# Kernel optimization log

Hardware: AMD Instinct MI355X
Metric: run time of the kernel (lower is better)

The kernel has to match this reference:

```python
import jax, jax.numpy as jnp
import numpy as np

N = 50000        # num_nodes
E = 800000       # num_edges (before self-loops)
F_IN = 64        # node_feature_dim
HID = 128        # hidden_dim per head (layer 1)
HEADS = 4
OUT = 256        # output_dim (layer 2, heads=1)
NEG_SLOPE = 0.2  # PyG GATConv default leaky_relu slope


def setup_inputs() -> dict:
    key = jax.random.key(0)
    ks = jax.random.split(key, 10)
    edge_index = jax.random.randint(ks[0], (2, E), 0, N, dtype=jnp.int32)
    node_emb = jax.random.normal(ks[1], (N, F_IN), jnp.float32)
    # Layer 1: GATConv(64 -> 128, heads=4, concat=True)
    W1 = jax.random.normal(ks[2], (F_IN, HEADS * HID), jnp.float32) / np.sqrt(F_IN)
    a_src1 = jax.random.normal(ks[3], (HEADS, HID), jnp.float32) / np.sqrt(HID)
    a_dst1 = jax.random.normal(ks[4], (HEADS, HID), jnp.float32) / np.sqrt(HID)
    b1 = jnp.zeros((HEADS * HID,), jnp.float32)
    # Layer 2: GATConv(512 -> 256, heads=1)
    W2 = jax.random.normal(ks[5], (HEADS * HID, OUT), jnp.float32) / np.sqrt(HEADS * HID)
    a_src2 = jax.random.normal(ks[6], (1, OUT), jnp.float32) / np.sqrt(OUT)
    a_dst2 = jax.random.normal(ks[7], (1, OUT), jnp.float32) / np.sqrt(OUT)
    b2 = jnp.zeros((OUT,), jnp.float32)
    return {
        "edge_index": edge_index, "node_emb": node_emb,
        "W1": W1, "a_src1": a_src1, "a_dst1": a_dst1, "b1": b1,
        "W2": W2, "a_src2": a_src2, "a_dst2": a_dst2, "b2": b2,
        "batch_size": 1,
    }


def gat_layer(x, src, dst, W, a_src, a_dst, b, heads, ch):
    """PyG-style GATConv (concat=True, self-loops already in src/dst)."""
    n = x.shape[0]
    xw = (x @ W).reshape(n, heads, ch)                       # [N, H, C]
    alpha_s = jnp.einsum('nhc,hc->nh', xw, a_src)            # [N, H]
    alpha_d = jnp.einsum('nhc,hc->nh', xw, a_dst)            # [N, H]
    logits = jax.nn.leaky_relu(alpha_s[src] + alpha_d[dst], NEG_SLOPE)  # [Etot, H]
    # numerically stable segment softmax over edges grouped by dst
    m = jax.ops.segment_max(logits, dst, num_segments=n)     # [N, H]
    e = jnp.exp(logits - m[dst])                             # [Etot, H]
    denom = jax.ops.segment_sum(e, dst, num_segments=n)      # [N, H]
    alpha = e / denom[dst]                                   # [Etot, H]
    msg = xw[src] * alpha[:, :, None]                        # [Etot, H, C]
    out = jax.ops.segment_sum(msg, dst, num_segments=n)      # [N, H, C]
    return out.reshape(n, heads * ch) + b


def reference(edge_index, node_emb, W1, a_src1, a_dst1, b1,
              W2, a_src2, a_dst2, b2, batch_size):
    # PyG GATConv adds self-loops by default
    loop = jnp.arange(N, dtype=edge_index.dtype)
    src = jnp.concatenate([edge_index[0], loop])
    dst = jnp.concatenate([edge_index[1], loop])
    x = gat_layer(node_emb, src, dst, W1, a_src1, a_dst1, b1, HEADS, HID)
    x = jax.nn.elu(x)                                        # dropout = identity (eval)
    x = gat_layer(x, src, dst, W2, a_src2, a_dst2, b2, 1, OUT)
    g = jnp.mean(x, axis=0, keepdims=True)                   # [1, OUT]
    if batch_size > 1:
        g = jnp.broadcast_to(g, (batch_size, OUT))
    return g
```

## Files before the change

kernel.cpp:

```cpp
#include <hip/hip_runtime.h>
#include <cstdint>
#include <cstddef>

#define NEG_SLOPE 0.2f

typedef __bf16 bf16x8 __attribute__((ext_vector_type(8)));
typedef __bf16 bf16x4 __attribute__((ext_vector_type(4)));
typedef float f32x4 __attribute__((ext_vector_type(4)));

__device__ __forceinline__ int dstKeyOf(const int* ei, int E, int i) {
  return (i < E) ? ei[E + i] : (i - E);
}
__device__ __forceinline__ int srcKeyOf(const int* ei, int E, int i) {
  return (i < E) ? ei[i] : (i - E);
}

__global__ __launch_bounds__(256) void prep_all_kernel(
    const float* __restrict__ W1, const float* __restrict__ as1, const float* __restrict__ ad1,
    const float* __restrict__ W2, const float* __restrict__ as2, const float* __restrict__ ad2,
    float* __restrict__ Vs, float* __restrict__ Vd,
    float* __restrict__ vs2, float* __restrict__ vd2,
    __bf16* __restrict__ W1T) {
  int bid = blockIdx.x, tid = threadIdx.x;
  if (bid == 0) {
    int k = tid >> 2, h = tid & 3;
    const float* w = W1 + k * 512 + h * 128;
    const float* a1 = as1 + h * 128;
    const float* a2 = ad1 + h * 128;
    float s = 0.f, d = 0.f;
    for (int c = 0; c < 128; ++c) { float wv = w[c]; s += wv * a1[c]; d += wv * a2[c]; }
    Vs[k * 4 + h] = s; Vd[k * 4 + h] = d;
  } else if (bid <= 2) {
    int k = (bid - 1) * 256 + tid;
    if (k < 512) {
      const float* w = W2 + k * 256;
      float s = 0.f, d = 0.f;
      for (int c = 0; c < 256; ++c) { float wv = w[c]; s += wv * as2[c]; d += wv * ad2[c]; }
      vs2[k] = s; vd2[k] = d;
    }
  } else {
    int idx = (bid - 3) * 256 + tid;
    int n = idx >> 6, k = idx & 63;
    W1T[idx] = (__bf16)W1[(size_t)k * 512 + n];
  }
}

__global__ void emb_prep_kernel(const float* __restrict__ emb, const float* __restrict__ Vs,
                                const float* __restrict__ Vd, __bf16* __restrict__ embb,
                                float* __restrict__ as_, float* __restrict__ ad_, int n) {
  __shared__ float sVs[256];
  __shared__ float sVd[256];
  for (int i = threadIdx.x; i < 256; i += blockDim.x) { sVs[i] = Vs[i]; sVd[i] = Vd[i]; }
  __syncthreads();
  int node = blockIdx.x * blockDim.x + threadIdx.x;
  if (node >= n) return;
  const float* xr = emb + (size_t)node * 64;
  __bf16* br = embb + (size_t)node * 64;
  float accs[4] = {}, accd[4] = {};
  for (int k = 0; k < 64; k += 4) {
    float4 xv = *(const float4*)(xr + k);
    bf16x4 o;
    o[0] = (__bf16)xv.x; o[1] = (__bf16)xv.y; o[2] = (__bf16)xv.z; o[3] = (__bf16)xv.w;
    *(bf16x4*)(br + k) = o;
#pragma unroll
    for (int h = 0; h < 4; ++h) {
      accs[h] += xv.x * sVs[(k + 0) * 4 + h] + xv.y * sVs[(k + 1) * 4 + h] +
                 xv.z * sVs[(k + 2) * 4 + h] + xv.w * sVs[(k + 3) * 4 + h];
      accd[h] += xv.x * sVd[(k + 0) * 4 + h] + xv.y * sVd[(k + 1) * 4 + h] +
                 xv.z * sVd[(k + 2) * 4 + h] + xv.w * sVd[(k + 3) * 4 + h];
    }
  }
#pragma unroll
  for (int h = 0; h < 4; ++h) {
    as_[(size_t)node * 4 + h] = accs[h];
    ad_[(size_t)node * 4 + h] = accd[h];
  }
}

__global__ __launch_bounds__(256) void hist_kernel(const int* __restrict__ ei, int E, int NT,
                                                   int nblk, int* __restrict__ hist) {
  __shared__ int h[256];
  int tid = threadIdx.x;
  h[tid] = 0;
  __syncthreads();
  int sec = (int)blockIdx.x >= nblk;
  int blk = blockIdx.x - sec * nblk;
  int base = blk * 1024;
#pragma unroll
  for (int j = 0; j < 4; ++j) {
    int i = base + j * 256 + tid;
    if (i < NT) {
      int key = sec ? srcKeyOf(ei, E, i) : dstKeyOf(ei, E, i);
      atomicAdd(&h[key >> 8], 1);
    }
  }
  __syncthreads();
  hist[(size_t)(sec * 256 + tid) * nblk + blk] = h[tid];
}

__global__ __launch_bounds__(1024) void exscan1_kernel(int* __restrict__ a, int* __restrict__ bsum,
                                                       int M) {
  __shared__ int ws[16];
  int t = threadIdx.x, lane = t & 63, w = t >> 6;
  int i = blockIdx.x * 1024 + t;
  int v = (i < M) ? a[i] : 0;
  int x = v;
#pragma unroll
  for (int s = 1; s < 64; s <<= 1) {
    int tt = __shfl_up(x, s, 64);
    if (lane >= s) x += tt;
  }
  if (lane == 63) ws[w] = x;
  __syncthreads();
  int wo = 0;
  for (int k = 0; k < w; ++k) wo += ws[k];
  if (i < M) a[i] = wo + x - v;
  if (t == 1023) bsum[blockIdx.x] = wo + x;
}

__global__ __launch_bounds__(512) void exscan2_kernel(int* __restrict__ bsum, int nb) {
  __shared__ int buf[512];
  int t = threadIdx.x;
  int v = (t < nb) ? bsum[t] : 0;
  buf[t] = v;
  __syncthreads();
  for (int s = 1; s < 512; s <<= 1) {
    int x = (t >= s) ? buf[t - s] : 0;
    __syncthreads();
    buf[t] += x;
    __syncthreads();
  }
  if (t < nb) bsum[t] = buf[t] - v;
}

__global__ __launch_bounds__(1024) void exscan3_kernel(int* __restrict__ a,
                                                       const int* __restrict__ bsum, int M) {
  int i = blockIdx.x * 1024 + threadIdx.x;
  if (i < M) a[i] += bsum[blockIdx.x];
}

__global__ __launch_bounds__(256) void scatter1_kernel(const int* __restrict__ ei, int E, int NT,
                                                       int nblk, const int* __restrict__ scanned,
                                                       int2* __restrict__ p1buf) {
  __shared__ int bins[256];
  int tid = threadIdx.x;
  int sec = (int)blockIdx.x >= nblk;
  int blk = blockIdx.x - sec * nblk;
  bins[tid] = scanned[(size_t)(sec * 256 + tid) * nblk + blk];
  __syncthreads();
  int base = blk * 1024;
#pragma unroll
  for (int j = 0; j < 4; ++j) {
    int i = base + j * 256 + tid;
    if (i < NT) {
      int k, p;
      if (sec == 0) { k = dstKeyOf(ei, E, i); p = srcKeyOf(ei, E, i); }
      else          { k = srcKeyOf(ei, E, i); p = dstKeyOf(ei, E, i); }
      int pos = atomicAdd(&bins[k >> 8], 1);
      p1buf[pos] = make_int2(k, p);
    }
  }
}

__global__ __launch_bounds__(1024) void sortlow_kernel(const int* __restrict__ scanned,
                                                       const int2* __restrict__ p1buf,
                                                       int nblk, int NT,
                                                       int* __restrict__ keyD, int* __restrict__ srcD,
                                                       int* __restrict__ keyS, int* __restrict__ dstS) {
  __shared__ int h[256];
  __shared__ int b2[256];
  int tid = threadIdx.x;
  int w = blockIdx.x;
  int sec = w >= 256;
  int d0 = w - sec * 256;
  int beg = scanned[(size_t)(sec * 256 + d0) * nblk];
  int end = (w == 511) ? 2 * NT : scanned[(size_t)(sec * 256 + d0 + 1) * nblk];
  if (tid < 256) h[tid] = 0;
  __syncthreads();
  for (int i = beg + tid; i < end; i += 1024) atomicAdd(&h[p1buf[i].x & 255], 1);
  __syncthreads();
  if (tid < 256) b2[tid] = h[tid];
  __syncthreads();
  for (int s = 1; s < 256; s <<= 1) {
    int x = (tid >= s && tid < 256) ? b2[tid - s] : 0;
    __syncthreads();
    if (tid < 256) b2[tid] += x;
    __syncthreads();
  }
  if (tid < 256) b2[tid] = beg + b2[tid] - h[tid];
  __syncthreads();
  for (int i = beg + tid; i < end; i += 1024) {
    int2 it = p1buf[i];
    int pos = atomicAdd(&b2[it.x & 255], 1);
    if (sec == 0) { keyD[pos] = it.x; srcD[pos] = it.y; }
    else          { keyS[pos - NT] = it.x; dstS[pos - NT] = it.y; }
  }
}

__global__ void bounds_kernel(const int* __restrict__ keyD, const int* __restrict__ keyS,
                              int* __restrict__ off, int* __restrict__ offS, int NT, int n) {
  int x = blockIdx.x * 256 + threadIdx.x;
  if (x == 0) { off[n] = NT; offS[n] = NT; }
  if (x >= 2 * n) return;
  int sec = x >= n;
  int d = x - sec * n;
  const int* key = sec ? keyS : keyD;
  int lo = 0, hi = NT;
  while (lo < hi) {
    int mid = (lo + hi) >> 1;
    if (key[mid] < d) lo = mid + 1; else hi = mid;
  }
  if (sec) offS[d] = lo; else off[d] = lo;
}

__global__ __launch_bounds__(128) void agg_emb_kernel(
    const int* __restrict__ off, const int* __restrict__ csr_src,
    const __bf16* __restrict__ embb, const float* __restrict__ as_,
    const float* __restrict__ ad_, __bf16* __restrict__ aggE) {
  int d = blockIdx.x * 2 + (threadIdx.x >> 6);
  int lane = threadIdx.x & 63;
  int g = lane >> 4, p = lane & 15;
  float4 adv = *(const float4*)(ad_ + (size_t)d * 4);
  float acc[4][4] = {};
  float wsum[4] = {};
  int beg = off[d], end = off[d + 1];
  for (int i0 = beg; i0 < end; i0 += 8) {
    int iA = i0 + g, iB = i0 + 4 + g;
    int idxA = (iA < end) ? iA : (end - 1);
    int idxB = (iB < end) ? iB : (end - 1);
    float vmA = (iA < end) ? 1.f : 0.f;
    float vmB = (iB < end) ? 1.f : 0.f;
    int sA = csr_src[idxA];
    int sB = csr_src[idxB];
    float4 aA = *(const float4*)(as_ + (size_t)sA * 4);
    float4 aB = *(const float4*)(as_ + (size_t)sB * 4);
    bf16x4 vA = *(const bf16x4*)(embb + (size_t)sA * 64 + p * 4);
    bf16x4 vB = *(const bf16x4*)(embb + (size_t)sB * 64 + p * 4);
    float lA0 = aA.x + adv.x; lA0 = lA0 >= 0.f ? lA0 : NEG_SLOPE * lA0;
    float lA1 = aA.y + adv.y; lA1 = lA1 >= 0.f ? lA1 : NEG_SLOPE * lA1;
    float lA2 = aA.z + adv.z; lA2 = lA2 >= 0.f ? lA2 : NEG_SLOPE * lA2;
    float lA3 = aA.w + adv.w; lA3 = lA3 >= 0.f ? lA3 : NEG_SLOPE * lA3;
    float lB0 = aB.x + adv.x; lB0 = lB0 >= 0.f ? lB0 : NEG_SLOPE * lB0;
    float lB1 = aB.y + adv.y; lB1 = lB1 >= 0.f ? lB1 : NEG_SLOPE * lB1;
    float lB2 = aB.z + adv.z; lB2 = lB2 >= 0.f ? lB2 : NEG_SLOPE * lB2;
    float lB3 = aB.w + adv.w; lB3 = lB3 >= 0.f ? lB3 : NEG_SLOPE * lB3;
    float wA0 = __expf(lA0) * vmA, wA1 = __expf(lA1) * vmA;
    float wA2 = __expf(lA2) * vmA, wA3 = __expf(lA3) * vmA;
    float wB0 = __expf(lB0) * vmB, wB1 = __expf(lB1) * vmB;
    float wB2 = __expf(lB2) * vmB, wB3 = __expf(lB3) * vmB;
    float fA0 = (float)vA[0], fA1 = (float)vA[1], fA2 = (float)vA[2], fA3 = (float)vA[3];
    float fB0 = (float)vB[0], fB1 = (float)vB[1], fB2 = (float)vB[2], fB3 = (float)vB[3];
    acc[0][0] += wA0 * fA0; acc[0][1] += wA0 * fA1; acc[0][2] += wA0 * fA2; acc[0][3] += wA0 * fA3;
    acc[1][0] += wA1 * fA0; acc[1][1] += wA1 * fA1; acc[1][2] += wA1 * fA2; acc[1][3] += wA1 * fA3;
    acc[2][0] += wA2 * fA0; acc[2][1] += wA2 * fA1; acc[2][2] += wA2 * fA2; acc[2][3] += wA2 * fA3;
    acc[3][0] += wA3 * fA0; acc[3][1] += wA3 * fA1; acc[3][2] += wA3 * fA2; acc[3][3] += wA3 * fA3;
    acc[0][0] += wB0 * fB0; acc[0][1] += wB0 * fB1; acc[0][2] += wB0 * fB2; acc[0][3] += wB0 * fB3;
    acc[1][0] += wB1 * fB0; acc[1][1] += wB1 * fB1; acc[1][2] += wB1 * fB2; acc[1][3] += wB1 * fB3;
    acc[2][0] += wB2 * fB0; acc[2][1] += wB2 * fB1; acc[2][2] += wB2 * fB2; acc[2][3] += wB2 * fB3;
    acc[3][0] += wB3 * fB0; acc[3][1] += wB3 * fB1; acc[3][2] += wB3 * fB2; acc[3][3] += wB3 * fB3;
    wsum[0] += wA0 + wB0; wsum[1] += wA1 + wB1; wsum[2] += wA2 + wB2; wsum[3] += wA3 + wB3;
  }
#pragma unroll
  for (int h = 0; h < 4; ++h) {
#pragma unroll
    for (int c = 0; c < 4; ++c) {
      acc[h][c] += __shfl_xor(acc[h][c], 16, 64);
      acc[h][c] += __shfl_xor(acc[h][c], 32, 64);
    }
    wsum[h] += __shfl_xor(wsum[h], 16, 64);
    wsum[h] += __shfl_xor(wsum[h], 32, 64);
  }
  if (g == 0) {
#pragma unroll
    for (int h = 0; h < 4; ++h) {
      float inv = 1.0f / wsum[h];
      bf16x4 o;
      o[0] = (__bf16)(acc[h][0] * inv); o[1] = (__bf16)(acc[h][1] * inv);
      o[2] = (__bf16)(acc[h][2] * inv); o[3] = (__bf16)(acc[h][3] * inv);
      *(bf16x4*)(aggE + (size_t)d * 256 + h * 64 + p * 4) = o;
    }
  }
}

__global__ __launch_bounds__(256) void gemm1p_kernel(const __bf16* __restrict__ aggE,
                                                     const __bf16* __restrict__ W1T,
                                                     const float* __restrict__ b1,
                                                     const float* __restrict__ vs2,
                                                     const float* __restrict__ vd2,
                                                     __bf16* __restrict__ x1,
                                                     float* __restrict__ as2p,
                                                     float* __restrict__ ad2p, int M) {
  __shared__ __bf16 Asl[128 * 72];
  __shared__ __bf16 Bsl[128 * 72];
  int tid = threadIdx.x;
  int h = blockIdx.z;
  int m0 = blockIdx.x * 128;
  int wave = tid >> 6, lane = tid & 63;
  int wm = (wave >> 1) * 64, wn = (wave & 1) * 64;
  int l15 = lane & 15, kg = lane >> 4;
#pragma unroll
  for (int i = 0; i < 4; ++i) {
    int c = tid + i * 256;
    int row = c >> 3, off = (c & 7) * 8;
    bf16x8 va = {};
    int gr = m0 + row;
    if (gr < M) va = *(const bf16x8*)(aggE + (size_t)gr * 256 + h * 64 + off);
    *(bf16x8*)(&Asl[row * 72 + off]) = va;
    bf16x8 vb = *(const bf16x8*)(W1T + ((size_t)h * 128 + row) * 64 + off);
    *(bf16x8*)(&Bsl[row * 72 + off]) = vb;
  }
  __syncthreads();
  f32x4 acc[4][4] = {};
#pragma unroll
  for (int ks = 0; ks < 2; ++ks) {
    bf16x8 af[4], bfr[4];
#pragma unroll
    for (int f = 0; f < 4; ++f) {
      af[f]  = *(const bf16x8*)(&Asl[(wm + f * 16 + l15) * 72 + kg * 8 + ks * 32]);
      bfr[f] = *(const bf16x8*)(&Bsl[(wn + f * 16 + l15) * 72 + kg * 8 + ks * 32]);
    }
#pragma unroll
    for (int i = 0; i < 4; ++i)
#pragma unroll
      for (int j = 0; j < 4; ++j)
        acc[i][j] = __builtin_amdgcn_mfma_f32_16x16x32_bf16(af[i], bfr[j], acc[i][j], 0, 0, 0);
  }
  float bv[4], vsv[4], vdv[4];
#pragma unroll
  for (int j = 0; j < 4; ++j) {
    int col = h * 128 + wn + j * 16 + l15;
    bv[j] = b1[col]; vsv[j] = vs2[col]; vdv[j] = vd2[col];
  }
  int slab = h * 2 + (wn >> 6);
#pragma unroll
  for (int i = 0; i < 4; ++i)
#pragma unroll
    for (int r = 0; r < 4; ++r) {
      int lrow = wm + i * 16 + kg * 4 + r;
      int row = m0 + lrow;
      bool vrow = row < M;
      float ps = 0.f, pd = 0.f;
#pragma unroll
      for (int j = 0; j < 4; ++j) {
        float a = acc[i][j][r] + bv[j];
        a = a > 0.f ? a : __expf(a) - 1.f;
        __bf16 xb = (__bf16)a;
        if (vrow) x1[(size_t)row * 512 + h * 128 + wn + j * 16 + l15] = xb;
        float af = (float)xb;
        ps += af * vsv[j];
        pd += af * vdv[j];
      }
      ps += __shfl_xor(ps, 1, 16); ps += __shfl_xor(ps, 2, 16);
      ps += __shfl_xor(ps, 4, 16); ps += __shfl_xor(ps, 8, 16);
      pd += __shfl_xor(pd, 1, 16); pd += __shfl_xor(pd, 2, 16);
      pd += __shfl_xor(pd, 4, 16); pd += __shfl_xor(pd, 8, 16);
      if (l15 == 0 && vrow) {
        as2p[(size_t)slab * M + row] = ps;
        ad2p[(size_t)slab * M + row] = pd;
      }
    }
}

__global__ void merge_alpha2_kernel(const float* __restrict__ as2p, const float* __restrict__ ad2p,
                                    float* __restrict__ as2, float* __restrict__ ad2, int n) {
  int i = blockIdx.x * blockDim.x + threadIdx.x;
  if (i >= n) return;
  float s = 0.f, d = 0.f;
#pragma unroll
  for (int b = 0; b < 8; ++b) {
    s += as2p[(size_t)b * n + i];
    d += ad2p[(size_t)b * n + i];
  }
  as2[i] = s; ad2[i] = d;
}

__global__ __launch_bounds__(256) void invw_kernel(
    const int* __restrict__ off, const int* __restrict__ csr_src,
    const float* __restrict__ as2, const float* __restrict__ ad2,
    float2* __restrict__ advw, float invN, int n) {
  int d = (blockIdx.x * 256 + threadIdx.x) >> 4;
  int p = threadIdx.x & 15;
  if (d >= n) return;
  float adv = ad2[d];
  int beg = off[d], end = off[d + 1];
  float wsum = 0.f;
  for (int i = beg + p; i < end; i += 16) {
    float l = as2[csr_src[i]] + adv;
    l = l >= 0.f ? l : NEG_SLOPE * l;
    wsum += __expf(l);
  }
  wsum += __shfl_xor(wsum, 1, 16); wsum += __shfl_xor(wsum, 2, 16);
  wsum += __shfl_xor(wsum, 4, 16); wsum += __shfl_xor(wsum, 8, 16);
  if (p == 0) advw[d] = make_float2(adv, invN / wsum);
}

__global__ __launch_bounds__(256) void gamma_csc_kernel(
    const int* __restrict__ offS, const int* __restrict__ csc_dst,
    const float* __restrict__ as2, const float2* __restrict__ advw,
    float* __restrict__ gamma, int n) {
  int s = (blockIdx.x * 256 + threadIdx.x) >> 4;
  int p = threadIdx.x & 15;
  if (s >= n) return;
  float as2s = as2[s];
  int beg = offS[s], end = offS[s + 1];
  float gsum = 0.f;
  for (int i = beg + p; i < end; i += 16) {
    float2 av = advw[csc_dst[i]];
    float l = as2s + av.x;
    l = l >= 0.f ? l : NEG_SLOPE * l;
    gsum += __expf(l) * av.y;
  }
  gsum += __shfl_xor(gsum, 1, 16); gsum += __shfl_xor(gsum, 2, 16);
  gsum += __shfl_xor(gsum, 4, 16); gsum += __shfl_xor(gsum, 8, 16);
  if (p == 0) gamma[s] = gsum;
}

__global__ __launch_bounds__(256) void colsum1_kernel(const __bf16* __restrict__ x1,
                                                      const float* __restrict__ gamma,
                                                      float* __restrict__ pcol, int n) {
  __shared__ float sc[512];
  int t = threadIdx.x;
  sc[t] = 0.f; sc[t + 256] = 0.f;
  __syncthreads();
  int lane = t & 63, w = t >> 6;
  float acc[8] = {};
  for (int r = blockIdx.x * 4 + w; r < n; r += gridDim.x * 4) {
    float g = gamma[r];
    bf16x8 v = *(const bf16x8*)(x1 + (size_t)r * 512 + lane * 8);
#pragma unroll
    for (int j = 0; j < 8; ++j) acc[j] += g * (float)v[j];
  }
#pragma unroll
  for (int j = 0; j < 8; ++j) atomicAdd(&sc[lane * 8 + j], acc[j]);
  __syncthreads();
  pcol[(size_t)blockIdx.x * 512 + t] = sc[t];
  pcol[(size_t)blockIdx.x * 512 + 256 + t] = sc[t + 256];
}

__global__ __launch_bounds__(256) void colsum2_kernel(const float* __restrict__ pcol,
                                                      float* __restrict__ colsum, int nb) {
  int c = threadIdx.x;
  int b0 = blockIdx.x * 16;
  float a0 = 0.f, a1 = 0.f;
#pragma unroll 4
  for (int b = b0; b < b0 + 16; ++b) {
    if (b < nb) {
      a0 += pcol[(size_t)b * 512 + c];
      a1 += pcol[(size_t)b * 512 + 256 + c];
    }
  }
  atomicAdd(&colsum[c], a0);
  atomicAdd(&colsum[c + 256], a1);
}

__global__ void final_kernel(const float* __restrict__ colsum, const float* __restrict__ W2,
                             const float* __restrict__ b2, float* __restrict__ out) {
  int c = threadIdx.x;
  int k0 = blockIdx.x * 64;
  float acc = 0.f;
  for (int k = k0; k < k0 + 64; ++k) acc += colsum[k] * W2[(size_t)k * 256 + c];
  if (blockIdx.x == 0) acc += b2[c];
  atomicAdd(&out[c], acc);
}

__global__ void bcast_kernel(float* __restrict__ dout, int total) {
  int i = blockIdx.x * blockDim.x + threadIdx.x;
  if (i >= 256 && i < total) dout[i] = dout[i & 255];
}

extern "C" void kernel_launch(void* const* d_in, const int* in_sizes, int n_in,
                              void* d_out, int out_size, void* d_ws, size_t ws_size,
                              hipStream_t stream) {
  const int* ei = (const int*)d_in[0];
  const float* emb = (const float*)d_in[1];
  const float* W1 = (const float*)d_in[2];
  const float* as1w = (const float*)d_in[3];
  const float* ad1w = (const float*)d_in[4];
  const float* b1 = (const float*)d_in[5];
  const float* W2 = (const float*)d_in[6];
  const float* as2w = (const float*)d_in[7];
  const float* ad2w = (const float*)d_in[8];
  const float* b2 = (const float*)d_in[9];
  float* out = (float*)d_out;

  const int E = in_sizes[0] / 2;
  const int N = in_sizes[1] / 64;
  const int NT = E + N;
  const int CS1 = 1024;
  const int nblk = (NT + 1023) / 1024;
  const int M = 2 * 256 * nblk;
  const int scanBlocks = (M + 1023) / 1024;

  char* ws = (char*)d_ws;
  size_t o = 0;
  auto alloc = [&](size_t bytes) { size_t r = o; o += (bytes + 255) & ~(size_t)255; return r; };
  __bf16* embb  = (__bf16*)(ws + alloc((size_t)N * 64 * 2));
  __bf16* aggE  = (__bf16*)(ws + alloc((size_t)N * 256 * 2));
  __bf16* x1    = (__bf16*)(ws + alloc((size_t)N * 512 * 2));
  __bf16* W1T   = (__bf16*)(ws + alloc((size_t)512 * 64 * 2));
  float* as1    = (float*)(ws + alloc((size_t)N * 4 * 4));
  float* ad1    = (float*)(ws + alloc((size_t)N * 4 * 4));
  float* as2    = (float*)(ws + alloc((size_t)N * 4));
  float* ad2    = (float*)(ws + alloc((size_t)N * 4));
  float* as2p   = (float*)(ws + alloc((size_t)8 * N * 4));
  float* ad2p   = (float*)(ws + alloc((size_t)8 * N * 4));
  float* pcol   = (float*)(ws + alloc((size_t)CS1 * 512 * 4));
  float2* advw  = (float2*)(ws + alloc((size_t)N * 8));
  float* gamma  = (float*)(ws + alloc((size_t)N * 4));
  int* off      = (int*)(ws + alloc((size_t)(N + 1) * 4));
  int* offS     = (int*)(ws + alloc((size_t)(N + 1) * 4));
  int* keyD     = (int*)(ws + alloc((size_t)NT * 4));
  int* srcD     = (int*)(ws + alloc((size_t)NT * 4));
  int* keyS     = (int*)(ws + alloc((size_t)NT * 4));
  int* dstS     = (int*)(ws + alloc((size_t)NT * 4));
  int2* p1buf   = (int2*)(ws + alloc((size_t)2 * NT * 8));
  int* hist     = (int*)(ws + alloc((size_t)M * 4));
  int* bsum     = (int*)(ws + alloc(512 * 4));
  size_t zbeg = o;
  float* colsum = (float*)(ws + alloc(512 * 4));
  size_t zend = o;
  float* Vs1    = (float*)(ws + alloc(64 * 4 * 4));
  float* Vd1    = (float*)(ws + alloc(64 * 4 * 4));
  float* vs2    = (float*)(ws + alloc(512 * 4));
  float* vd2    = (float*)(ws + alloc(512 * 4));

  hipMemsetAsync(ws + zbeg, 0, zend - zbeg, stream);
  hipMemsetAsync(d_out, 0, (size_t)out_size * 4, stream);

  prep_all_kernel<<<131, 256, 0, stream>>>(W1, as1w, ad1w, W2, as2w, ad2w,
                                           Vs1, Vd1, vs2, vd2, W1T);
  int nb = (N + 255) / 256;
  emb_prep_kernel<<<nb, 256, 0, stream>>>(emb, Vs1, Vd1, embb, as1, ad1, N);

  hist_kernel<<<2 * nblk, 256, 0, stream>>>(ei, E, NT, nblk, hist);
  exscan1_kernel<<<scanBlocks, 1024, 0, stream>>>(hist, bsum, M);
  exscan2_kernel<<<1, 512, 0, stream>>>(bsum, scanBlocks);
  exscan3_kernel<<<scanBlocks, 1024, 0, stream>>>(hist, bsum, M);
  scatter1_kernel<<<2 * nblk, 256, 0, stream>>>(ei, E, NT, nblk, hist, p1buf);
  sortlow_kernel<<<512, 1024, 0, stream>>>(hist, p1buf, nblk, NT, keyD, srcD, keyS, dstS);
  bounds_kernel<<<(2 * N + 255) / 256, 256, 0, stream>>>(keyD, keyS, off, offS, NT, N);

  agg_emb_kernel<<<N / 2, 128, 0, stream>>>(off, srcD, embb, as1, ad1, aggE);
  dim3 g1((N + 127) / 128, 1, 4);
  gemm1p_kernel<<<g1, 256, 0, stream>>>(aggE, W1T, b1, vs2, vd2, x1, as2p, ad2p, N);
  merge_alpha2_kernel<<<nb, 256, 0, stream>>>(as2p, ad2p, as2, ad2, N);

  invw_kernel<<<(N * 16 + 255) / 256, 256, 0, stream>>>(off, srcD, as2, ad2, advw,
                                                        1.0f / (float)N, N);
  gamma_csc_kernel<<<(N * 16 + 255) / 256, 256, 0, stream>>>(offS, dstS, as2, advw, gamma, N);
  colsum1_kernel<<<CS1, 256, 0, stream>>>(x1, gamma, pcol, N);
  colsum2_kernel<<<CS1 / 16, 256, 0, stream>>>(pcol, colsum, CS1);
  final_kernel<<<8, 256, 0, stream>>>(colsum, W2, b2, out);

  if (out_size > 256) {
    bcast_kernel<<<(out_size + 255) / 256, 256, 0, stream>>>(out, out_size);
  }
}
```

Before: 204.2 us.

## Fuse histogram into prep kernel, drop scan pass, precompute edge weights

Three changes. The histogram pass now runs as extra blocks of the prep kernel. The third scan pass is removed by adding the block sums on the fly wherever scanned values are read. The layer-1 edge exponentials are computed in a new kernel that shares a launch with the CSR bounds search, so agg_emb_kernel only loads a float4 weight per edge instead of gathering attention scores and evaluating exp. This cuts kernel launches and arithmetic in the aggregation, but adds a 16-byte-per-edge buffer that is written once and read back.

```diff
diff --git a/kernel.cpp b/kernel.cpp
--- a/kernel.cpp
+++ b/kernel.cpp
@@ -15,12 +15,13 @@
   return (i < E) ? ei[i] : (i - E);
 }
 
-__global__ __launch_bounds__(256) void prep_all_kernel(
+__global__ __launch_bounds__(256) void prep_front_kernel(
     const float* __restrict__ W1, const float* __restrict__ as1, const float* __restrict__ ad1,
     const float* __restrict__ W2, const float* __restrict__ as2, const float* __restrict__ ad2,
+    const int* __restrict__ ei, int E, int NT, int nblk,
     float* __restrict__ Vs, float* __restrict__ Vd,
     float* __restrict__ vs2, float* __restrict__ vd2,
-    __bf16* __restrict__ W1T) {
+    __bf16* __restrict__ W1T, int* __restrict__ hist) {
   int bid = blockIdx.x, tid = threadIdx.x;
   if (bid == 0) {
     int k = tid >> 2, h = tid & 3;
@@ -38,10 +39,28 @@
       for (int c = 0; c < 256; ++c) { float wv = w[c]; s += wv * as2[c]; d += wv * ad2[c]; }
       vs2[k] = s; vd2[k] = d;
     }
-  } else {
+  } else if (bid <= 130) {
     int idx = (bid - 3) * 256 + tid;
     int n = idx >> 6, k = idx & 63;
     W1T[idx] = (__bf16)W1[(size_t)k * 512 + n];
+  } else {
+    __shared__ int h[256];
+    h[tid] = 0;
+    __syncthreads();
+    int hblk = bid - 131;
+    int sec = hblk >= nblk;
+    int blk = hblk - sec * nblk;
+    int base = blk * 1024;
+#pragma unroll
+    for (int j = 0; j < 4; ++j) {
+      int i = base + j * 256 + tid;
+      if (i < NT) {
+        int key = sec ? srcKeyOf(ei, E, i) : dstKeyOf(ei, E, i);
+        atomicAdd(&h[key >> 8], 1);
+      }
+    }
+    __syncthreads();
+    hist[(size_t)(sec * 256 + tid) * nblk + blk] = h[tid];
   }
 }
 
@@ -77,27 +96,6 @@
   }
 }
 
-__global__ __launch_bounds__(256) void hist_kernel(const int* __restrict__ ei, int E, int NT,
-                                                   int nblk, int* __restrict__ hist) {
-  __shared__ int h[256];
-  int tid = threadIdx.x;
-  h[tid] = 0;
-  __syncthreads();
-  int sec = (int)blockIdx.x >= nblk;
-  int blk = blockIdx.x - sec * nblk;
-  int base = blk * 1024;
-#pragma unroll
-  for (int j = 0; j < 4; ++j) {
-    int i = base + j * 256 + tid;
-    if (i < NT) {
-      int key = sec ? srcKeyOf(ei, E, i) : dstKeyOf(ei, E, i);
-      atomicAdd(&h[key >> 8], 1);
-    }
-  }
-  __syncthreads();
-  hist[(size_t)(sec * 256 + tid) * nblk + blk] = h[tid];
-}
-
 __global__ __launch_bounds__(1024) void exscan1_kernel(int* __restrict__ a, int* __restrict__ bsum,
                                                        int M) {
   __shared__ int ws[16];
@@ -133,20 +131,19 @@
   if (t < nb) bsum[t] = buf[t] - v;
 }
 
-__global__ __launch_bounds__(1024) void exscan3_kernel(int* __restrict__ a,
-                                                       const int* __restrict__ bsum, int M) {
-  int i = blockIdx.x * 1024 + threadIdx.x;
-  if (i < M) a[i] += bsum[blockIdx.x];
+__device__ __forceinline__ int scannedAt(const int* hist, const int* bsum, size_t idx) {
+  return hist[idx] + bsum[idx >> 10];
 }
 
 __global__ __launch_bounds__(256) void scatter1_kernel(const int* __restrict__ ei, int E, int NT,
-                                                       int nblk, const int* __restrict__ scanned,
+                                                       int nblk, const int* __restrict__ hist,
+                                                       const int* __restrict__ bsum,
                                                        int2* __restrict__ p1buf) {
   __shared__ int bins[256];
   int tid = threadIdx.x;
   int sec = (int)blockIdx.x >= nblk;
   int blk = blockIdx.x - sec * nblk;
-  bins[tid] = scanned[(size_t)(sec * 256 + tid) * nblk + blk];
+  bins[tid] = scannedAt(hist, bsum, (size_t)(sec * 256 + tid) * nblk + blk);
   __syncthreads();
   int base = blk * 1024;
 #pragma unroll
@@ -162,7 +159,8 @@
   }
 }
 
-__global__ __launch_bounds__(1024) void sortlow_kernel(const int* __restrict__ scanned,
+__global__ __launch_bounds__(1024) void sortlow_kernel(const int* __restrict__ hist,
+                                                       const int* __restrict__ bsum,
                                                        const int2* __restrict__ p1buf,
                                                        int nblk, int NT,
                                                        int* __restrict__ keyD, int* __restrict__ srcD,
@@ -173,8 +171,8 @@
   int w = blockIdx.x;
   int sec = w >= 256;
   int d0 = w - sec * 256;
-  int beg = scanned[(size_t)(sec * 256 + d0) * nblk];
-  int end = (w == 511) ? 2 * NT : scanned[(size_t)(sec * 256 + d0 + 1) * nblk];
+  int beg = scannedAt(hist, bsum, (size_t)(sec * 256 + d0) * nblk);
+  int end = (w == 511) ? 2 * NT : scannedAt(hist, bsum, (size_t)(sec * 256 + d0 + 1) * nblk);
   if (tid < 256) h[tid] = 0;
   __syncthreads();
   for (int i = beg + tid; i < end; i += 1024) atomicAdd(&h[p1buf[i].x & 255], 1);
@@ -197,30 +195,45 @@
   }
 }
 
-__global__ void bounds_kernel(const int* __restrict__ keyD, const int* __restrict__ keyS,
-                              int* __restrict__ off, int* __restrict__ offS, int NT, int n) {
-  int x = blockIdx.x * 256 + threadIdx.x;
-  if (x == 0) { off[n] = NT; offS[n] = NT; }
-  if (x >= 2 * n) return;
-  int sec = x >= n;
-  int d = x - sec * n;
-  const int* key = sec ? keyS : keyD;
-  int lo = 0, hi = NT;
-  while (lo < hi) {
-    int mid = (lo + hi) >> 1;
-    if (key[mid] < d) lo = mid + 1; else hi = mid;
-  }
-  if (sec) offS[d] = lo; else off[d] = lo;
+__global__ __launch_bounds__(256) void post_sort_kernel(
+    const int* __restrict__ keyD, const int* __restrict__ srcD, const int* __restrict__ keyS,
+    const float* __restrict__ as1, const float* __restrict__ ad1,
+    float4* __restrict__ ew4, int* __restrict__ off, int* __restrict__ offS,
+    int NT, int n, int ewBlocks) {
+  if ((int)blockIdx.x < ewBlocks) {
+    int i = blockIdx.x * 256 + threadIdx.x;
+    if (i >= NT) return;
+    int s = srcD[i], d = keyD[i];
+    float4 a = *(const float4*)(as1 + (size_t)s * 4);
+    float4 b = *(const float4*)(ad1 + (size_t)d * 4);
+    float l0 = a.x + b.x; l0 = l0 >= 0.f ? l0 : NEG_SLOPE * l0;
+    float l1 = a.y + b.y; l1 = l1 >= 0.f ? l1 : NEG_SLOPE * l1;
+    float l2 = a.z + b.z; l2 = l2 >= 0.f ? l2 : NEG_SLOPE * l2;
+    float l3 = a.w + b.w; l3 = l3 >= 0.f ? l3 : NEG_SLOPE * l3;
+    ew4[i] = make_float4(__expf(l0), __expf(l1), __expf(l2), __expf(l3));
+  } else {
+    int x = (blockIdx.x - ewBlocks) * 256 + threadIdx.x;
+    if (x == 0) { off[n] = NT; offS[n] = NT; }
+    if (x >= 2 * n) return;
+    int sec = x >= n;
+    int d = x - sec * n;
+    const int* key = sec ? keyS : keyD;
+    int lo = 0, hi = NT;
+    while (lo < hi) {
+      int mid = (lo + hi) >> 1;
+      if (key[mid] < d) lo = mid + 1; else hi = mid;
+    }
+    if (sec) offS[d] = lo; else off[d] = lo;
+  }
 }
 
 __global__ __launch_bounds__(128) void agg_emb_kernel(
-    const int* __restrict__ off, const int* __restrict__ csr_src,
-    const __bf16* __restrict__ embb, const float* __restrict__ as_,
-    const float* __restrict__ ad_, __bf16* __restrict__ aggE) {
+    const int* __restrict__ off, const int* __restrict__ srcD,
+    const float4* __restrict__ ew4, const __bf16* __restrict__ embb,
+    __bf16* __restrict__ aggE) {
   int d = blockIdx.x * 2 + (threadIdx.x >> 6);
   int lane = threadIdx.x & 63;
   int g = lane >> 4, p = lane & 15;
-  float4 adv = *(const float4*)(ad_ + (size_t)d * 4);
   float acc[4][4] = {};
   float wsum[4] = {};
   int beg = off[d], end = off[d + 1];
@@ -230,24 +243,14 @@
     int idxB = (iB < end) ? iB : (end - 1);
     float vmA = (iA < end) ? 1.f : 0.f;
     float vmB = (iB < end) ? 1.f : 0.f;
-    int sA = csr_src[idxA];
-    int sB = csr_src[idxB];
-    float4 aA = *(const float4*)(as_ + (size_t)sA * 4);
-    float4 aB = *(const float4*)(as_ + (size_t)sB * 4);
+    int sA = srcD[idxA];
+    int sB = srcD[idxB];
+    float4 wAv = ew4[idxA];
+    float4 wBv = ew4[idxB];
     bf16x4 vA = *(const bf16x4*)(embb + (size_t)sA * 64 + p * 4);
     bf16x4 vB = *(const bf16x4*)(embb + (size_t)sB * 64 + p * 4);
-    float lA0 = aA.x + adv.x; lA0 = lA0 >= 0.f ? lA0 : NEG_SLOPE * lA0;
-    float lA1 = aA.y + adv.y; lA1 = lA1 >= 0.f ? lA1 : NEG_SLOPE * lA1;
-    float lA2 = aA.z + adv.z; lA2 = lA2 >= 0.f ? lA2 : NEG_SLOPE * lA2;
-    float lA3 = aA.w + adv.w; lA3 = lA3 >= 0.f ? lA3 : NEG_SLOPE * lA3;
-    float lB0 = aB.x + adv.x; lB0 = lB0 >= 0.f ? lB0 : NEG_SLOPE * lB0;
-    float lB1 = aB.y + adv.y; lB1 = lB1 >= 0.f ? lB1 : NEG_SLOPE * lB1;
-    float lB2 = aB.z + adv.z; lB2 = lB2 >= 0.f ? lB2 : NEG_SLOPE * lB2;
-    float lB3 = aB.w + adv.w; lB3 = lB3 >= 0.f ? lB3 : NEG_SLOPE * lB3;
-    float wA0 = __expf(lA0) * vmA, wA1 = __expf(lA1) * vmA;
-    float wA2 = __expf(lA2) * vmA, wA3 = __expf(lA3) * vmA;
-    float wB0 = __expf(lB0) * vmB, wB1 = __expf(lB1) * vmB;
-    float wB2 = __expf(lB2) * vmB, wB3 = __expf(lB3) * vmB;
+    float wA0 = wAv.x * vmA, wA1 = wAv.y * vmA, wA2 = wAv.z * vmA, wA3 = wAv.w * vmA;
+    float wB0 = wBv.x * vmB, wB1 = wBv.y * vmB, wB2 = wBv.z * vmB, wB3 = wBv.w * vmB;
     float fA0 = (float)vA[0], fA1 = (float)vA[1], fA2 = (float)vA[2], fA3 = (float)vA[3];
     float fB0 = (float)vB[0], fB1 = (float)vB[1], fB2 = (float)vB[2], fB3 = (float)vB[3];
     acc[0][0] += wA0 * fA0; acc[0][1] += wA0 * fA1; acc[0][2] += wA0 * fA2; acc[0][3] += wA0 * fA3;
@@ -516,6 +519,7 @@
   int2* p1buf   = (int2*)(ws + alloc((size_t)2 * NT * 8));
   int* hist     = (int*)(ws + alloc((size_t)M * 4));
   int* bsum     = (int*)(ws + alloc(512 * 4));
+  float4* ew4   = (float4*)(ws + alloc((size_t)NT * 16));
   size_t zbeg = o;
   float* colsum = (float*)(ws + alloc(512 * 4));
   size_t zend = o;
@@ -527,20 +531,23 @@
   hipMemsetAsync(ws + zbeg, 0, zend - zbeg, stream);
   hipMemsetAsync(d_out, 0, (size_t)out_size * 4, stream);
 
-  prep_all_kernel<<<131, 256, 0, stream>>>(W1, as1w, ad1w, W2, as2w, ad2w,
-                                           Vs1, Vd1, vs2, vd2, W1T);
+  prep_front_kernel<<<131 + 2 * nblk, 256, 0, stream>>>(W1, as1w, ad1w, W2, as2w, ad2w,
+                                                        ei, E, NT, nblk,
+                                                        Vs1, Vd1, vs2, vd2, W1T, hist);
   int nb = (N + 255) / 256;
   emb_prep_kernel<<<nb, 256, 0, stream>>>(emb, Vs1, Vd1, embb, as1, ad1, N);
 
-  hist_kernel<<<2 * nblk, 256, 0, stream>>>(ei, E, NT, nblk, hist);
   exscan1_kernel<<<scanBlocks, 1024, 0, stream>>>(hist, bsum, M);
   exscan2_kernel<<<1, 512, 0, stream>>>(bsum, scanBlocks);
-  exscan3_kernel<<<scanBlocks, 1024, 0, stream>>>(hist, bsum, M);
-  scatter1_kernel<<<2 * nblk, 256, 0, stream>>>(ei, E, NT, nblk, hist, p1buf);
-  sortlow_kernel<<<512, 1024, 0, stream>>>(hist, p1buf, nblk, NT, keyD, srcD, keyS, dstS);
-  bounds_kernel<<<(2 * N + 255) / 256, 256, 0, stream>>>(keyD, keyS, off, offS, NT, N);
-
-  agg_emb_kernel<<<N / 2, 128, 0, stream>>>(off, srcD, embb, as1, ad1, aggE);
+  scatter1_kernel<<<2 * nblk, 256, 0, stream>>>(ei, E, NT, nblk, hist, bsum, p1buf);
+  sortlow_kernel<<<512, 1024, 0, stream>>>(hist, bsum, p1buf, nblk, NT, keyD, srcD, keyS, dstS);
+
+  int ewBlocks = (NT + 255) / 256;
+  int bBlocks = (2 * N + 255) / 256;
+  post_sort_kernel<<<ewBlocks + bBlocks, 256, 0, stream>>>(keyD, srcD, keyS, as1, ad1,
+                                                           ew4, off, offS, NT, N, ewBlocks);
+
+  agg_emb_kernel<<<N / 2, 128, 0, stream>>>(off, srcD, ew4, embb, aggE);
   dim3 g1((N + 127) / 128, 1, 4);
   gemm1p_kernel<<<g1, 256, 0, stream>>>(aggE, W1T, b1, vs2, vd2, x1, as2p, ad2p, N);
   merge_alpha2_kernel<<<nb, 256, 0, stream>>>(as2p, ad2p, as2, ad2, N);
```

Result: faster. 197.1 us (-3.5%).
